# Performance work log

Hardware: AMD Instinct MI355X
Metric: run time of the kernel (lower is better)

## Reference

```python
import jax, jax.numpy as jnp
import numpy as np

D_MODEL = 1024
NUM_HEADS = 16
D_K = D_MODEL // NUM_HEADS  # 64


def _xavier(key, shape):
    fan_in, fan_out = shape[-1], shape[-2]
    limit = float(np.sqrt(6.0 / (fan_in + fan_out)))
    return jax.random.uniform(key, shape, jnp.float32, -limit, limit)


def setup_inputs() -> dict:
    key = jax.random.key(0)
    kx, kq, kk, kv, ko = jax.random.split(key, 5)
    x = jax.random.normal(kx, (2, 2048, D_MODEL), dtype=jnp.float32)
    q_heads = _xavier(kq, (NUM_HEADS, D_K, D_MODEL))
    k_heads = _xavier(kk, (NUM_HEADS, D_K, D_MODEL))
    v_heads = _xavier(kv, (NUM_HEADS, D_K, D_MODEL))
    output_proj = _xavier(ko, (D_MODEL, NUM_HEADS * D_K))
    return {"x": x, "q_heads": q_heads, "k_heads": k_heads,
            "v_heads": v_heads, "output_proj": output_proj}


def reference(x, q_heads, k_heads, v_heads, output_proj):
    # x: [b, s, d]; q/k/v_heads: [h, dk, d]; output_proj: [d, h*dk]
    b, s, d = x.shape
    h, dk, _ = q_heads.shape
    scale = 1.0 / jnp.sqrt(jnp.asarray(dk, x.dtype))
    # per-head projections: [b, h, s, dk]
    Q = jnp.einsum('bsd,hkd->bhsk', x, q_heads)
    K = jnp.einsum('bsd,hkd->bhsk', x, k_heads)
    V = jnp.einsum('bsd,hkd->bhsk', x, v_heads)
    scores = jnp.einsum('bhqk,bhsk->bhqs', Q, K) * scale  # [b,h,s,s]
    causal = jnp.tril(jnp.ones((s, s), dtype=bool))       # True where allowed
    scores = jnp.where(causal, scores, -jnp.inf)
    attn = jax.nn.softmax(scores, axis=-1)
    out = jnp.einsum('bhqs,bhsk->bhqk', attn, V)           # [b,h,s,dk]
    out = out.transpose(0, 2, 1, 3).reshape(b, s, h * dk)  # [b,s,h*dk]
    return jnp.einsum('bsk,dk->bsd', out, output_proj)
```

## Files before the change

### kernel.cpp

```cpp
#include <hip/hip_runtime.h>
#include <hip/hip_bf16.h>
#include <math.h>

#define D_MODEL 1024
#define NHEADS  16
#define DK      64
#define SEQ     2048
#define KDIM    1024

typedef __bf16 bf16x8 __attribute__((ext_vector_type(8)));
typedef float  f32x4  __attribute__((ext_vector_type(4)));

__device__ __forceinline__ void gload16(const void* g, void* l) {
    __builtin_amdgcn_global_load_lds(
        (const __attribute__((address_space(1))) void*)g,
        (__attribute__((address_space(3))) void*)l, 16, 0, 0);
}

__device__ __forceinline__ unsigned short f2bf(float f) {
    __hip_bfloat16 h = __float2bfloat16(f);
    return *(unsigned short*)&h;
}

__global__ __launch_bounds__(256) void cast_kernel(
    const float* __restrict__ x,
    const float* __restrict__ qw,
    const float* __restrict__ kw,
    const float* __restrict__ vw,
    const float* __restrict__ wo,
    unsigned short* __restrict__ xb,
    unsigned short* __restrict__ wqkv,
    unsigned short* __restrict__ wob)
{
    const size_t t = (size_t)blockIdx.x * 256 + threadIdx.x;
    const size_t X4 = 1048576;
    const size_t W4 = 262144;

    const float* src;
    unsigned short* dst;
    size_t o;
    if (t < X4)            { src = x;  dst = xb;             o = t; }
    else if (t < X4 + W4)  { src = qw; dst = wqkv;           o = t - X4; }
    else if (t < X4 + 2*W4){ src = kw; dst = wqkv + 1048576; o = t - X4 - W4; }
    else if (t < X4 + 3*W4){ src = vw; dst = wqkv + 2097152; o = t - X4 - 2*W4; }
    else                   { src = wo; dst = wob;            o = t - X4 - 3*W4; }

    float4 v = ((const float4*)src)[o];
    ushort4 r;
    r.x = f2bf(v.x); r.y = f2bf(v.y); r.z = f2bf(v.z); r.w = f2bf(v.w);
    ((ushort4*)dst)[o] = r;
}

template<int MODE>
__global__ __launch_bounds__(256) void mfma_gemm(
    const unsigned short* __restrict__ A,
    const unsigned short* __restrict__ B,
    float* __restrict__ C0,
    unsigned short* __restrict__ Qb,
    unsigned short* __restrict__ Kb,
    unsigned short* __restrict__ Vtb)
{
    __shared__ unsigned short As[128 * 32];
    __shared__ unsigned short Bs[128 * 32];

    const int tid  = threadIdx.x;
    const int wave = tid >> 6;
    const int lane = tid & 63;
    const int wr   = wave >> 1;
    const int wc   = wave & 1;
    const int quad = lane >> 4;
    const int l16  = lane & 15;

    const int rowBase = blockIdx.y * 128;
    const int colBase = blockIdx.x * 128;

    f32x4 acc[4][4];
    const f32x4 z = {0.f, 0.f, 0.f, 0.f};
#pragma unroll
    for (int i = 0; i < 4; ++i)
#pragma unroll
        for (int j = 0; j < 4; ++j) acc[i][j] = z;

    const int srow = lane >> 2;
    const int skof = (lane & 3) * 8;

    for (int k0 = 0; k0 < KDIM; k0 += 32) {
        __syncthreads();

        const unsigned short* ga =
            A + (size_t)(rowBase + wave * 32) * KDIM + k0;
        gload16(ga + (size_t)srow * KDIM + skof,        &As[(wave*32)    * 32]);
        gload16(ga + (size_t)(16 + srow) * KDIM + skof, &As[(wave*32+16) * 32]);

        const unsigned short* gb =
            B + (size_t)(colBase + wave * 32) * KDIM + k0;
        gload16(gb + (size_t)srow * KDIM + skof,        &Bs[(wave*32)    * 32]);
        gload16(gb + (size_t)(16 + srow) * KDIM + skof, &Bs[(wave*32+16) * 32]);

        __syncthreads();

        bf16x8 af[4], bfr[4];
#pragma unroll
        for (int t = 0; t < 4; ++t)
            af[t] = *(const bf16x8*)&As[(wr*64 + t*16 + l16) * 32 + quad*8];
#pragma unroll
        for (int t = 0; t < 4; ++t)
            bfr[t] = *(const bf16x8*)&Bs[(wc*64 + t*16 + l16) * 32 + quad*8];

#pragma unroll
        for (int tr = 0; tr < 4; ++tr)
#pragma unroll
            for (int tc = 0; tc < 4; ++tc)
                acc[tr][tc] = __builtin_amdgcn_mfma_f32_16x16x32_bf16(
                    af[tr], bfr[tc], acc[tr][tc], 0, 0, 0);
    }

#pragma unroll
    for (int tr = 0; tr < 4; ++tr) {
#pragma unroll
        for (int tc = 0; tc < 4; ++tc) {
            const int grow0 = rowBase + wr*64 + tr*16 + quad*4;
            const int gcol  = colBase + wc*64 + tc*16 + l16;
            if (MODE == 0) {
                const int m  = gcol >> 10;
                const int kk = gcol & 1023;
                const int h  = kk >> 6, dk = kk & 63;
                const int b  = grow0 >> 11, s0 = grow0 & (SEQ - 1);
                if (m == 2) {
                    ushort4 pk;
                    pk.x = f2bf(acc[tr][tc][0]); pk.y = f2bf(acc[tr][tc][1]);
                    pk.z = f2bf(acc[tr][tc][2]); pk.w = f2bf(acc[tr][tc][3]);
                    *(ushort4*)(Vtb + ((size_t)(b*NHEADS + h)*DK + dk)*SEQ + s0) = pk;
                } else {
                    unsigned short* dst = (m == 0 ? Qb : Kb);
#pragma unroll
                    for (int reg = 0; reg < 4; ++reg)
                        dst[((size_t)(b*NHEADS + h)*SEQ + s0 + reg)*DK + dk] =
                            f2bf(acc[tr][tc][reg]);
                }
            } else {
#pragma unroll
                for (int reg = 0; reg < 4; ++reg)
                    C0[(size_t)(grow0 + reg) * D_MODEL + gcol] = acc[tr][tc][reg];
            }
        }
    }
}

__global__ __launch_bounds__(256) void attn_mfma_kernel(
    const unsigned short* __restrict__ Qb,
    const unsigned short* __restrict__ Kb,
    const unsigned short* __restrict__ Vtb,
    unsigned short* __restrict__ O)
{
    __shared__ unsigned short Ks[64 * 64];
    __shared__ unsigned short Vs[64 * 64];
    __shared__ unsigned short Ps[4 * 16 * 64];

    const int bh   = blockIdx.x;
    const int qt   = 31 - blockIdx.y;
    const int wave = threadIdx.x >> 6;
    const int lane = threadIdx.x & 63;
    const int quad = lane >> 4;
    const int l16  = lane & 15;

    const size_t qrow = (size_t)bh * SEQ + qt*64 + wave*16 + l16;
    bf16x8 aq0 = *(const bf16x8*)(Qb + qrow * DK + quad*8);
    bf16x8 aq1 = *(const bf16x8*)(Qb + qrow * DK + 32 + quad*8);

    f32x4 o_acc[4];
    const f32x4 z = {0.f, 0.f, 0.f, 0.f};
#pragma unroll
    for (int i = 0; i < 4; ++i) o_acc[i] = z;
    float mrow = -1e30f, lrow = 0.f;

    const int srow8  = lane >> 3;
    const int schunk = lane & 7;
    const unsigned short* Kbase = Kb  + (size_t)bh * SEQ * DK;
    const unsigned short* Vbase = Vtb + (size_t)bh * DK * SEQ;
    const float scale = 0.125f;

    const int ntiles = qt + 1;
    for (int jt = 0; jt < ntiles; ++jt) {
        const int j0 = jt * 64;
        __syncthreads();
#pragma unroll
        for (int n = 0; n < 2; ++n) {
            const int r = wave*16 + n*8 + srow8;
            gload16(Kbase + (size_t)(j0 + r) * DK + (schunk ^ srow8) * 8,
                    &Ks[(wave*16 + n*8) * 64]);
            gload16(Vbase + (size_t)r * SEQ + j0 + (schunk ^ srow8) * 8,
                    &Vs[(wave*16 + n*8) * 64]);
        }
        __syncthreads();

        f32x4 st[4];
#pragma unroll
        for (int ct = 0; ct < 4; ++ct) {
            const int r = ct*16 + l16;
            bf16x8 k0 = *(const bf16x8*)&Ks[r*64 + ((quad     ^ (r&7)) * 8)];
            bf16x8 k1 = *(const bf16x8*)&Ks[r*64 + (((4+quad) ^ (r&7)) * 8)];
            f32x4 t = z;
            t = __builtin_amdgcn_mfma_f32_16x16x32_bf16(k0, aq0, t, 0, 0, 0);
            t = __builtin_amdgcn_mfma_f32_16x16x32_bf16(k1, aq1, t, 0, 0, 0);
            st[ct] = t;
        }

        if (jt == qt) {
#pragma unroll
            for (int ct = 0; ct < 4; ++ct)
#pragma unroll
                for (int reg = 0; reg < 4; ++reg) {
                    const int kl = ct*16 + quad*4 + reg;
                    const int ql = wave*16 + l16;
                    st[ct][reg] = (kl <= ql) ? st[ct][reg] * scale : -1e30f;
                }
        } else {
#pragma unroll
            for (int ct = 0; ct < 4; ++ct)
#pragma unroll
                for (int reg = 0; reg < 4; ++reg) st[ct][reg] *= scale;
        }

        float mx = st[0][0];
#pragma unroll
        for (int ct = 0; ct < 4; ++ct)
#pragma unroll
            for (int reg = 0; reg < 4; ++reg) mx = fmaxf(mx, st[ct][reg]);
        mx = fmaxf(mx, __shfl_xor(mx, 16));
        mx = fmaxf(mx, __shfl_xor(mx, 32));

        const float mnew  = fmaxf(mrow, mx);
        const float alpha = __expf(mrow - mnew);
        mrow = mnew;

        float rs = 0.f;
#pragma unroll
        for (int ct = 0; ct < 4; ++ct)
#pragma unroll
            for (int reg = 0; reg < 4; ++reg) {
                float p = __expf(st[ct][reg] - mnew);
                st[ct][reg] = p;
                rs += p;
            }
        rs += __shfl_xor(rs, 16);
        rs += __shfl_xor(rs, 32);
        lrow = lrow * alpha + rs;
#pragma unroll
        for (int ot = 0; ot < 4; ++ot) {
            o_acc[ot][0] *= alpha; o_acc[ot][1] *= alpha;
            o_acc[ot][2] *= alpha; o_acc[ot][3] *= alpha;
        }

        unsigned short* Pw = &Ps[wave * 1024];
#pragma unroll
        for (int ct = 0; ct < 4; ++ct) {
            ushort4 pk;
            pk.x = f2bf(st[ct][0]); pk.y = f2bf(st[ct][1]);
            pk.z = f2bf(st[ct][2]); pk.w = f2bf(st[ct][3]);
            const int g = (ct*4 + quad) ^ ((l16 & 7) << 1);
            *(ushort4*)(Pw + l16*64 + g*4) = pk;
        }

        bf16x8 bp0 = *(const bf16x8*)(Pw + l16*64 + ((quad     ^ (l16&7)) * 8));
        bf16x8 bp1 = *(const bf16x8*)(Pw + l16*64 + (((4+quad) ^ (l16&7)) * 8));

#pragma unroll
        for (int ot = 0; ot < 4; ++ot) {
            const int r = ot*16 + l16;
            bf16x8 v0 = *(const bf16x8*)&Vs[r*64 + ((quad     ^ (r&7)) * 8)];
            bf16x8 v1 = *(const bf16x8*)&Vs[r*64 + (((4+quad) ^ (r&7)) * 8)];
            o_acc[ot] = __builtin_amdgcn_mfma_f32_16x16x32_bf16(v0, bp0, o_acc[ot], 0, 0, 0);
            o_acc[ot] = __builtin_amdgcn_mfma_f32_16x16x32_bf16(v1, bp1, o_acc[ot], 0, 0, 0);
        }
    }

    const float inv = 1.f / lrow;
    const int b = bh >> 4, h = bh & 15;
    const int sg = qt*64 + wave*16 + l16;
    unsigned short* orow = O + ((size_t)(b * SEQ + sg)) * D_MODEL + h * DK;
#pragma unroll
    for (int ot = 0; ot < 4; ++ot) {
        ushort4 pk;
        pk.x = f2bf(o_acc[ot][0] * inv); pk.y = f2bf(o_acc[ot][1] * inv);
        pk.z = f2bf(o_acc[ot][2] * inv); pk.w = f2bf(o_acc[ot][3] * inv);
        *(ushort4*)(orow + ot*16 + quad*4) = pk;
    }
}

extern "C" void kernel_launch(void* const* d_in, const int* in_sizes, int n_in,
                              void* d_out, int out_size, void* d_ws, size_t ws_size,
                              hipStream_t stream) {
    const float* x  = (const float*)d_in[0];
    const float* qw = (const float*)d_in[1];
    const float* kw = (const float*)d_in[2];
    const float* vw = (const float*)d_in[3];
    const float* wo = (const float*)d_in[4];
    float* out = (float*)d_out;

    char* ws = (char*)d_ws;
    unsigned short* Qb   = (unsigned short*)(ws);
    unsigned short* Kb   = (unsigned short*)(ws + (size_t) 8*1024*1024);
    unsigned short* Vtb  = (unsigned short*)(ws + (size_t)16*1024*1024);
    unsigned short* AO   = (unsigned short*)(ws + (size_t)24*1024*1024);
    unsigned short* XB   = (unsigned short*)(ws + (size_t)32*1024*1024);
    unsigned short* WQKV = (unsigned short*)(ws + (size_t)40*1024*1024);
    unsigned short* WOB  = (unsigned short*)(ws + (size_t)46*1024*1024);

    cast_kernel<<<8192, 256, 0, stream>>>(x, qw, kw, vw, wo, XB, WQKV, WOB);

    dim3 g1(24, 32);
    mfma_gemm<0><<<g1, 256, 0, stream>>>(XB, WQKV, nullptr, Qb, Kb, Vtb);

    dim3 g2(32, 32);
    attn_mfma_kernel<<<g2, 256, 0, stream>>>(Qb, Kb, Vtb, AO);

    dim3 g3(8, 32);
    mfma_gemm<1><<<g3, 256, 0, stream>>>(AO, WOB, out, nullptr, nullptr, nullptr);
}
```

Measured before the change: 185.3 us.

## Use 128-row query tiles in attention, fold scale into Q, use exp2

The attention kernel now gives each block 128 query rows, with two 16-row sub-tiles per wave, so every K/V tile loaded into LDS feeds twice as many MFMAs. The softmax scale times log2(e) is folded into Q when the projection GEMM writes it, which lets the inner loop use exp2f with no per-element multiply. Rescaling of the output accumulator is skipped when no row maximum changed, and fully masked sub-tiles skip compute. In exchange the grid has half as many blocks, register pressure is higher, and the per-wave P buffer in LDS doubles.

```diff
diff --git a/kernel.cpp b/kernel.cpp
--- a/kernel.cpp
+++ b/kernel.cpp
@@ -21,6 +21,8 @@
     __hip_bfloat16 h = __float2bfloat16(f);
     return *(unsigned short*)&h;
 }
+
+#define QSCALE 0.18033688011112042f
 
 __global__ __launch_bounds__(256) void cast_kernel(
     const float* __restrict__ x,
@@ -133,10 +135,11 @@
                     *(ushort4*)(Vtb + ((size_t)(b*NHEADS + h)*DK + dk)*SEQ + s0) = pk;
                 } else {
                     unsigned short* dst = (m == 0 ? Qb : Kb);
+                    const float sc = (m == 0) ? QSCALE : 1.0f;
 #pragma unroll
                     for (int reg = 0; reg < 4; ++reg)
                         dst[((size_t)(b*NHEADS + h)*SEQ + s0 + reg)*DK + dk] =
-                            f2bf(acc[tr][tc][reg]);
+                            f2bf(acc[tr][tc][reg] * sc);
                 }
             } else {
 #pragma unroll
@@ -155,32 +158,40 @@
 {
     __shared__ unsigned short Ks[64 * 64];
     __shared__ unsigned short Vs[64 * 64];
-    __shared__ unsigned short Ps[4 * 16 * 64];
+    __shared__ unsigned short Ps[4 * 32 * 64];
 
     const int bh   = blockIdx.x;
-    const int qt   = 31 - blockIdx.y;
+    const int qt   = 15 - blockIdx.y;
     const int wave = threadIdx.x >> 6;
     const int lane = threadIdx.x & 63;
     const int quad = lane >> 4;
     const int l16  = lane & 15;
-
-    const size_t qrow = (size_t)bh * SEQ + qt*64 + wave*16 + l16;
-    bf16x8 aq0 = *(const bf16x8*)(Qb + qrow * DK + quad*8);
-    bf16x8 aq1 = *(const bf16x8*)(Qb + qrow * DK + 32 + quad*8);
-
-    f32x4 o_acc[4];
+    const int q0   = qt*128 + wave*32;
+
+    bf16x8 aq[2][2];
+#pragma unroll
+    for (int qs = 0; qs < 2; ++qs) {
+        const size_t qrow = (size_t)bh * SEQ + q0 + qs*16 + l16;
+        aq[qs][0] = *(const bf16x8*)(Qb + qrow * DK + quad*8);
+        aq[qs][1] = *(const bf16x8*)(Qb + qrow * DK + 32 + quad*8);
+    }
+
+    f32x4 o_acc[2][4];
     const f32x4 z = {0.f, 0.f, 0.f, 0.f};
 #pragma unroll
-    for (int i = 0; i < 4; ++i) o_acc[i] = z;
-    float mrow = -1e30f, lrow = 0.f;
+    for (int qs = 0; qs < 2; ++qs)
+#pragma unroll
+        for (int i = 0; i < 4; ++i) o_acc[qs][i] = z;
+    float m2[2] = {-1e30f, -1e30f};
+    float l2[2] = {0.f, 0.f};
 
     const int srow8  = lane >> 3;
     const int schunk = lane & 7;
     const unsigned short* Kbase = Kb  + (size_t)bh * SEQ * DK;
     const unsigned short* Vbase = Vtb + (size_t)bh * DK * SEQ;
-    const float scale = 0.125f;
-
-    const int ntiles = qt + 1;
+    unsigned short* Pw = &Ps[wave * 2048];
+
+    const int ntiles = 2*qt + 2;
     for (int jt = 0; jt < ntiles; ++jt) {
         const int j0 = jt * 64;
         __syncthreads();
@@ -194,97 +205,134 @@
         }
         __syncthreads();
 
-        f32x4 st[4];
-#pragma unroll
-        for (int ct = 0; ct < 4; ++ct) {
-            const int r = ct*16 + l16;
-            bf16x8 k0 = *(const bf16x8*)&Ks[r*64 + ((quad     ^ (r&7)) * 8)];
-            bf16x8 k1 = *(const bf16x8*)&Ks[r*64 + (((4+quad) ^ (r&7)) * 8)];
-            f32x4 t = z;
-            t = __builtin_amdgcn_mfma_f32_16x16x32_bf16(k0, aq0, t, 0, 0, 0);
-            t = __builtin_amdgcn_mfma_f32_16x16x32_bf16(k1, aq1, t, 0, 0, 0);
-            st[ct] = t;
+        if (j0 <= q0 + 31) {
+            f32x4 st[2][4];
+#pragma unroll
+            for (int ct = 0; ct < 4; ++ct) {
+                const int r = ct*16 + l16;
+                bf16x8 k0 = *(const bf16x8*)&Ks[r*64 + ((quad     ^ (r&7)) * 8)];
+                bf16x8 k1 = *(const bf16x8*)&Ks[r*64 + (((4+quad) ^ (r&7)) * 8)];
+#pragma unroll
+                for (int qs = 0; qs < 2; ++qs) {
+                    f32x4 t = z;
+                    t = __builtin_amdgcn_mfma_f32_16x16x32_bf16(k0, aq[qs][0], t, 0, 0, 0);
+                    t = __builtin_amdgcn_mfma_f32_16x16x32_bf16(k1, aq[qs][1], t, 0, 0, 0);
+                    st[qs][ct] = t;
+                }
+            }
+
+            if (j0 + 63 > q0) {
+#pragma unroll
+                for (int qs = 0; qs < 2; ++qs)
+#pragma unroll
+                    for (int ct = 0; ct < 4; ++ct)
+#pragma unroll
+                        for (int reg = 0; reg < 4; ++reg) {
+                            const int kl = j0 + ct*16 + quad*4 + reg;
+                            const int ql = q0 + qs*16 + l16;
+                            if (kl > ql) st[qs][ct][reg] = -1e30f;
+                        }
+            }
+
+            float mx[2];
+#pragma unroll
+            for (int qs = 0; qs < 2; ++qs) {
+                float m_ = st[qs][0][0];
+#pragma unroll
+                for (int ct = 0; ct < 4; ++ct)
+#pragma unroll
+                    for (int reg = 0; reg < 4; ++reg)
+                        m_ = fmaxf(m_, st[qs][ct][reg]);
+                m_ = fmaxf(m_, __shfl_xor(m_, 16));
+                m_ = fmaxf(m_, __shfl_xor(m_, 32));
+                mx[qs] = m_;
+            }
+
+            const float mn0 = fmaxf(m2[0], mx[0]);
+            const float mn1 = fmaxf(m2[1], mx[1]);
+            if (__any((mx[0] > m2[0]) | (mx[1] > m2[1]))) {
+                const float a0 = exp2f(m2[0] - mn0);
+                const float a1 = exp2f(m2[1] - mn1);
+                m2[0] = mn0; m2[1] = mn1;
+                l2[0] *= a0; l2[1] *= a1;
+#pragma unroll
+                for (int ot = 0; ot < 4; ++ot) {
+#pragma unroll
+                    for (int reg = 0; reg < 4; ++reg) {
+                        o_acc[0][ot][reg] *= a0;
+                        o_acc[1][ot][reg] *= a1;
+                    }
+                }
+            }
+
+#pragma unroll
+            for (int qs = 0; qs < 2; ++qs) {
+                float rs = 0.f;
+#pragma unroll
+                for (int ct = 0; ct < 4; ++ct)
+#pragma unroll
+                    for (int reg = 0; reg < 4; ++reg) {
+                        float p = exp2f(st[qs][ct][reg] - m2[qs]);
+                        st[qs][ct][reg] = p;
+                        rs += p;
+                    }
+                rs += __shfl_xor(rs, 16);
+                rs += __shfl_xor(rs, 32);
+                l2[qs] += rs;
+            }
+
+#pragma unroll
+            for (int qs = 0; qs < 2; ++qs) {
+                const int row = qs*16 + l16;
+#pragma unroll
+                for (int ct = 0; ct < 4; ++ct) {
+                    ushort4 pk;
+                    pk.x = f2bf(st[qs][ct][0]); pk.y = f2bf(st[qs][ct][1]);
+                    pk.z = f2bf(st[qs][ct][2]); pk.w = f2bf(st[qs][ct][3]);
+                    const int g = (ct*4 + quad) ^ ((row & 7) << 1);
+                    *(ushort4*)(Pw + row*64 + g*4) = pk;
+                }
+            }
+
+            bf16x8 bp[2][2];
+#pragma unroll
+            for (int qs = 0; qs < 2; ++qs) {
+                const int row = qs*16 + l16;
+                bp[qs][0] = *(const bf16x8*)(Pw + row*64 + ((quad     ^ (row&7)) * 8));
+                bp[qs][1] = *(const bf16x8*)(Pw + row*64 + (((4+quad) ^ (row&7)) * 8));
+            }
+
+#pragma unroll
+            for (int ot = 0; ot < 4; ++ot) {
+                const int r = ot*16 + l16;
+                bf16x8 v0 = *(const bf16x8*)&Vs[r*64 + ((quad     ^ (r&7)) * 8)];
+                bf16x8 v1 = *(const bf16x8*)&Vs[r*64 + (((4+quad) ^ (r&7)) * 8)];
+#pragma unroll
+                for (int qs = 0; qs < 2; ++qs) {
+                    o_acc[qs][ot] = __builtin_amdgcn_mfma_f32_16x16x32_bf16(
+                        v0, bp[qs][0], o_acc[qs][ot], 0, 0, 0);
+                    o_acc[qs][ot] = __builtin_amdgcn_mfma_f32_16x16x32_bf16(
+                        v1, bp[qs][1], o_acc[qs][ot], 0, 0, 0);
+                }
+            }
         }
-
-        if (jt == qt) {
-#pragma unroll
-            for (int ct = 0; ct < 4; ++ct)
-#pragma unroll
-                for (int reg = 0; reg < 4; ++reg) {
-                    const int kl = ct*16 + quad*4 + reg;
-                    const int ql = wave*16 + l16;
-                    st[ct][reg] = (kl <= ql) ? st[ct][reg] * scale : -1e30f;
-                }
-        } else {
-#pragma unroll
-            for (int ct = 0; ct < 4; ++ct)
-#pragma unroll
-                for (int reg = 0; reg < 4; ++reg) st[ct][reg] *= scale;
+    }
+
+    const int b = bh >> 4, h = bh & 15;
+#pragma unroll
+    for (int qs = 0; qs < 2; ++qs) {
+        const float inv = 1.f / l2[qs];
+        const int sg = q0 + qs*16 + l16;
+        unsigned short* orow = O + ((size_t)(b * SEQ + sg)) * D_MODEL + h * DK;
+#pragma unroll
+        for (int ot = 0; ot < 4; ++ot) {
+            ushort4 pk;
+            pk.x = f2bf(o_acc[qs][ot][0] * inv);
+            pk.y = f2bf(o_acc[qs][ot][1] * inv);
+            pk.z = f2bf(o_acc[qs][ot][2] * inv);
+            pk.w = f2bf(o_acc[qs][ot][3] * inv);
+            *(ushort4*)(orow + ot*16 + quad*4) = pk;
         }
-
-        float mx = st[0][0];
-#pragma unroll
-        for (int ct = 0; ct < 4; ++ct)
-#pragma unroll
-            for (int reg = 0; reg < 4; ++reg) mx = fmaxf(mx, st[ct][reg]);
-        mx = fmaxf(mx, __shfl_xor(mx, 16));
-        mx = fmaxf(mx, __shfl_xor(mx, 32));
-
-        const float mnew  = fmaxf(mrow, mx);
-        const float alpha = __expf(mrow - mnew);
-        mrow = mnew;
-
-        float rs = 0.f;
-#pragma unroll
-        for (int ct = 0; ct < 4; ++ct)
-#pragma unroll
-            for (int reg = 0; reg < 4; ++reg) {
-                float p = __expf(st[ct][reg] - mnew);
-                st[ct][reg] = p;
-                rs += p;
-            }
-        rs += __shfl_xor(rs, 16);
-        rs += __shfl_xor(rs, 32);
-        lrow = lrow * alpha + rs;
-#pragma unroll
-        for (int ot = 0; ot < 4; ++ot) {
-            o_acc[ot][0] *= alpha; o_acc[ot][1] *= alpha;
-            o_acc[ot][2] *= alpha; o_acc[ot][3] *= alpha;
-        }
-
-        unsigned short* Pw = &Ps[wave * 1024];
-#pragma unroll
-        for (int ct = 0; ct < 4; ++ct) {
-            ushort4 pk;
-            pk.x = f2bf(st[ct][0]); pk.y = f2bf(st[ct][1]);
-            pk.z = f2bf(st[ct][2]); pk.w = f2bf(st[ct][3]);
-            const int g = (ct*4 + quad) ^ ((l16 & 7) << 1);
-            *(ushort4*)(Pw + l16*64 + g*4) = pk;
-        }
-
-        bf16x8 bp0 = *(const bf16x8*)(Pw + l16*64 + ((quad     ^ (l16&7)) * 8));
-        bf16x8 bp1 = *(const bf16x8*)(Pw + l16*64 + (((4+quad) ^ (l16&7)) * 8));
-
-#pragma unroll
-        for (int ot = 0; ot < 4; ++ot) {
-            const int r = ot*16 + l16;
-            bf16x8 v0 = *(const bf16x8*)&Vs[r*64 + ((quad     ^ (r&7)) * 8)];
-            bf16x8 v1 = *(const bf16x8*)&Vs[r*64 + (((4+quad) ^ (r&7)) * 8)];
-            o_acc[ot] = __builtin_amdgcn_mfma_f32_16x16x32_bf16(v0, bp0, o_acc[ot], 0, 0, 0);
-            o_acc[ot] = __builtin_amdgcn_mfma_f32_16x16x32_bf16(v1, bp1, o_acc[ot], 0, 0, 0);
-        }
-    }
-
-    const float inv = 1.f / lrow;
-    const int b = bh >> 4, h = bh & 15;
-    const int sg = qt*64 + wave*16 + l16;
-    unsigned short* orow = O + ((size_t)(b * SEQ + sg)) * D_MODEL + h * DK;
-#pragma unroll
-    for (int ot = 0; ot < 4; ++ot) {
-        ushort4 pk;
-        pk.x = f2bf(o_acc[ot][0] * inv); pk.y = f2bf(o_acc[ot][1] * inv);
-        pk.z = f2bf(o_acc[ot][2] * inv); pk.w = f2bf(o_acc[ot][3] * inv);
-        *(ushort4*)(orow + ot*16 + quad*4) = pk;
     }
 }
 
@@ -312,7 +360,7 @@
     dim3 g1(24, 32);
     mfma_gemm<0><<<g1, 256, 0, stream>>>(XB, WQKV, nullptr, Qb, Kb, Vtb);
 
-    dim3 g2(32, 32);
+    dim3 g2(32, 16);
     attn_mfma_kernel<<<g2, 256, 0, stream>>>(Qb, Kb, Vtb, AO);
 
     dim3 g3(8, 32);
```

Result: slower. 209.0 us (+12.7%).
